# Performance work log

Measured on AMD Instinct MI355X. Metric: run time of the kernel, lower is better.

Reference implementation:

```python
import jax, jax.numpy as jnp
import numpy as np

DT = 0.1
WHEELBASE = 2.8
STATE_DIM = 12


def setup_inputs() -> dict:
    key = jax.random.key(0)
    k1, k2, k3 = jax.random.split(key, 3)
    b, l, h = 512, 64, 80
    x0 = jax.random.normal(k1, (b, STATE_DIM), dtype=jnp.float32)
    controls = jax.random.normal(k2, (b, l, h, 3), dtype=jnp.float32)
    deg = jax.random.uniform(k3, (b, 5), dtype=jnp.float32)
    return {"x0": x0, "controls": controls, "deg": deg}


def reference(x0, controls, deg):
    b, l, h, _ = controls.shape
    # degradation scales, broadcast over the l (candidate) dim: [b, 1]
    steer_scale = jnp.maximum(deg[:, 0:1], 0.05)
    brake_scale = jnp.maximum(deg[:, 1:2], 0.05)
    throttle_scale = jnp.maximum(deg[:, 2:3], 0.05)
    friction = jnp.maximum(deg[:, 4:5], 0.1)

    x_init = jnp.broadcast_to(x0[:, None, :], (b, l, x0.shape[-1]))  # [b,l,12]

    def step(x, u):  # x: [b,l,12], u: [b,l,3]
        delta = steer_scale * jnp.tanh(u[..., 0])
        fb = brake_scale * jax.nn.sigmoid(u[..., 1])
        fx = throttle_scale * jax.nn.sigmoid(u[..., 2])
        px, py, psi, vx, vy = (x[..., 0], x[..., 1], x[..., 2], x[..., 3], x[..., 4])
        speed = jnp.sqrt(vx * vx + vy * vy + 1e-06)
        acc = jnp.minimum(jnp.maximum(2.8 * fx - 6.5 * fb, -7.5 * friction), 3.0)
        speed2 = jnp.maximum(speed + acc * DT, 0.0)
        tan_d = jnp.tan(jnp.clip(delta, -0.75, 0.75))
        raw_yaw = speed2 / WHEELBASE * tan_d
        yaw_lim = jnp.maximum(friction * 9.81 / jnp.maximum(speed2, 2.0), 0.15)
        yaw_rate = jnp.clip(raw_yaw, -1.0, 1.0) * yaw_lim
        beta = jnp.clip(jnp.arctan(0.45 * tan_d), -0.65, 0.65)
        psi2 = psi + yaw_rate * DT
        vx2 = speed2 * jnp.cos(psi2 + beta)
        vy2 = speed2 * jnp.sin(psi2 + beta)
        px2 = px + vx2 * DT
        py2 = py + vy2 * DT
        ax = (vx2 - vx) / DT
        ay = (vy2 - vy) / DT
        x2 = jnp.stack([px2, py2, psi2, vx2, vy2, yaw_rate, ax, ay, beta, delta, fb, fx], -1)
        return x2, x2

    controls_t = jnp.moveaxis(controls, 2, 0)  # [h,b,l,3]
    _, traj = jax.lax.scan(step, x_init, controls_t)  # traj: [h,b,l,12]
    traj = jnp.concatenate([x_init[None], traj], axis=0)  # [h+1,b,l,12]
    return jnp.moveaxis(traj, 0, 2)  # [b,l,h+1,12]
```

## Files before the change

### kernel.cpp

```cpp
#include <hip/hip_runtime.h>
#include <math.h>


#define N_B 512
#define N_L 64
#define N_H 80
#define DT_F 0.1f
#define PITCH_F4 25
#define CPITCH 7
#define SPC 8
#define NCH 10
#define INV2PI 0.15915494309189535f

__device__ __forceinline__ float fast_rcp(float x) { return __builtin_amdgcn_rcpf(x); }

__device__ __forceinline__ float fast_tanh(float x) {
    const float e2 = __expf(2.0f * x);
    return (e2 - 1.0f) * fast_rcp(e2 + 1.0f);
}

__device__ __forceinline__ float fast_sigmoid(float x) {
    return fast_rcp(1.0f + __expf(-x));
}

__device__ __forceinline__ float fast_atan_small(float z) {
    const float z2 = z * z;
    float p = 1.0f / 9.0f;
    p = fmaf(p, z2, -1.0f / 7.0f);
    p = fmaf(p, z2, 1.0f / 5.0f);
    p = fmaf(p, z2, -1.0f / 3.0f);
    p = fmaf(p, z2, 1.0f);
    return z * p;
}

__device__ __forceinline__ float fast_tan_075(float x) {
    const float x2 = x * x;
    float p = 0.0035916f;
    p = fmaf(p, x2, 0.0088632f);
    p = fmaf(p, x2, 0.0218695f);
    p = fmaf(p, x2, 0.0539683f);
    p = fmaf(p, x2, 0.1333333f);
    p = fmaf(p, x2, 0.3333333f);
    return fmaf(p * x2, x, x);
}

struct Ctl { float delta, fb, fx, tan_d, beta, acc; };

__device__ __forceinline__ Ctl make_ctl(float u0, float u1, float u2,
                                        float steer_scale, float brake_scale,
                                        float throttle_scale, float neg_brake_lim) {
    Ctl t;
    t.delta = steer_scale * fast_tanh(u0);
    t.fb = brake_scale    * fast_sigmoid(u1);
    t.fx = throttle_scale * fast_sigmoid(u2);
    const float dc = fminf(fmaxf(t.delta, -0.75f), 0.75f);
    t.tan_d = fast_tan_075(dc);
    t.beta = fminf(fmaxf(fast_atan_small(0.45f * t.tan_d), -0.65f), 0.65f);
    t.acc = fminf(fmaxf(2.8f * t.fx - 6.5f * t.fb, neg_brake_lim), 3.0f);
    return t;
}

__global__ __launch_bounds__(128) void degraded_bicycle_rollout_kernel(
    const float* __restrict__ x0,
    const float* __restrict__ controls,
    const float* __restrict__ deg,
    float* __restrict__ out)
{
    __shared__ float4 lds4[2][N_L * PITCH_F4];
    __shared__ float4 ldsc[2][N_L * CPITCH];

    const int lane = threadIdx.x & 63;
    const int wave = threadIdx.x >> 6;
    const int b = blockIdx.x;

    const size_t out_b = (size_t)b * 62208;

#define FLUSH_SLICE(FBUF, FC)                                                     \
    {                                                                             \
        const size_t obase = out_b + 12 + (size_t)(FC) * (SPC * 12);              \
        _Pragma("unroll")                                                         \
        for (int i = 0; i < 24; ++i) {                                            \
            const unsigned flat = i * 64 + lane;                                  \
            const unsigned l = flat / 24u;                                        \
            const unsigned q = flat - l * 24u;                                    \
            const float4 v = lds4[FBUF][l * PITCH_F4 + q];                        \
            *reinterpret_cast<float4*>(out + obase + (size_t)l * 972 + q * 4) = v;\
        }                                                                         \
    }

#define CTL_L(i) (((i) * 64u + (unsigned)lane) / 6u)
#define CTL_J(i) (((i) * 64u + (unsigned)lane) - CTL_L(i) * 6u)

    if (wave == 0) {
        const float* dg = deg + b * 5;
        const float steer_scale    = fmaxf(dg[0], 0.05f);
        const float brake_scale    = fmaxf(dg[1], 0.05f);
        const float throttle_scale = fmaxf(dg[2], 0.05f);
        const float friction       = fmaxf(dg[4], 0.1f);

        const float4* x0v = reinterpret_cast<const float4*>(x0 + b * 12);
        const float4 xi0 = x0v[0];
        const float4 xi1 = x0v[1];

        float px  = xi0.x;
        float py  = xi0.y;
        float psi = xi0.z;
        float vxp = xi0.w;
        float vyp = xi1.x;
        float s = __builtin_amdgcn_sqrtf(fmaf(vxp, vxp, fmaf(vyp, vyp, 1e-6f)));

        const float neg_brake_lim = -7.5f * friction;
        const float yaw_num = friction * 9.81f;
        const float inv_wheelbase = 1.0f / 2.8f;

        __syncthreads();

        for (int c = 0; c < NCH; ++c) {
            float4* lrow = &lds4[c & 1][lane * PITCH_F4];
            const float4* crow = &ldsc[c & 1][lane * CPITCH];

            const float4 u0 = crow[0];
            const float4 u1 = crow[1];
            const float4 u2 = crow[2];
            const float4 u3 = crow[3];
            const float4 u4 = crow[4];
            const float4 u5 = crow[5];

            const Ctl tA = make_ctl(u0.x, u0.y, u0.z, steer_scale, brake_scale, throttle_scale, neg_brake_lim);
            const Ctl tB = make_ctl(u0.w, u1.x, u1.y, steer_scale, brake_scale, throttle_scale, neg_brake_lim);
            const Ctl tC = make_ctl(u1.z, u1.w, u2.x, steer_scale, brake_scale, throttle_scale, neg_brake_lim);
            const Ctl tD = make_ctl(u2.y, u2.z, u2.w, steer_scale, brake_scale, throttle_scale, neg_brake_lim);
            const Ctl tE = make_ctl(u3.x, u3.y, u3.z, steer_scale, brake_scale, throttle_scale, neg_brake_lim);
            const Ctl tF = make_ctl(u3.w, u4.x, u4.y, steer_scale, brake_scale, throttle_scale, neg_brake_lim);
            const Ctl tG = make_ctl(u4.z, u4.w, u5.x, steer_scale, brake_scale, throttle_scale, neg_brake_lim);
            const Ctl tH = make_ctl(u5.y, u5.z, u5.w, steer_scale, brake_scale, throttle_scale, neg_brake_lim);

#define ROLL_STEP(T, RR)                                                          \
            {                                                                     \
                const float s2 = fmaxf(fmaf((T).acc, DT_F, s), 0.0f);             \
                const float raw_yaw = s2 * inv_wheelbase * (T).tan_d;             \
                const float yaw_lim = fmaxf(yaw_num * fast_rcp(fmaxf(s2, 2.0f)), 0.15f); \
                const float yaw_rate = fminf(fmaxf(raw_yaw, -1.0f), 1.0f) * yaw_lim; \
                const float psi2 = fmaf(yaw_rate, DT_F, psi);                     \
                const float ang = (psi2 + (T).beta) * INV2PI;                     \
                const float sn = __builtin_amdgcn_sinf(ang);                      \
                const float cs = __builtin_amdgcn_cosf(ang);                      \
                const float vx2 = s2 * cs;                                        \
                const float vy2 = s2 * sn;                                        \
                const float px2 = fmaf(vx2, DT_F, px);                            \
                const float py2 = fmaf(vy2, DT_F, py);                            \
                const float ax = (vx2 - vxp) * 10.0f;                             \
                const float ay = (vy2 - vyp) * 10.0f;                             \
                lrow[(RR) * 3 + 0] = make_float4(px2, py2, psi2, vx2);            \
                lrow[(RR) * 3 + 1] = make_float4(vy2, yaw_rate, ax, ay);          \
                lrow[(RR) * 3 + 2] = make_float4((T).beta, (T).delta, (T).fb, (T).fx); \
                s = __builtin_amdgcn_sqrtf(fmaf(s2, s2, 1e-6f));                  \
                px = px2; py = py2; psi = psi2; vxp = vx2; vyp = vy2;             \
            }

            ROLL_STEP(tA, 0) ROLL_STEP(tB, 1) ROLL_STEP(tC, 2) ROLL_STEP(tD, 3)
            ROLL_STEP(tE, 4) ROLL_STEP(tF, 5) ROLL_STEP(tG, 6) ROLL_STEP(tH, 7)
#undef ROLL_STEP

            __syncthreads();
        }
    } else {
        {
            const float4* x0v = reinterpret_cast<const float4*>(x0 + b * 12);
            const float4 xq0 = x0v[0];
            const float4 xq1 = x0v[1];
            const float4 xq2 = x0v[2];
            #pragma unroll
            for (int i = 0; i < 3; ++i) {
                const unsigned flat = i * 64 + lane;
                const unsigned l = flat / 3u;
                const unsigned q = flat - l * 3u;
                const float4 v = (q == 0) ? xq0 : (q == 1) ? xq1 : xq2;
                *reinterpret_cast<float4*>(out + out_b + (size_t)l * 972 + q * 4) = v;
            }
        }
        {
            const size_t gbase = (size_t)b * 15360;
            float4 q0 = *reinterpret_cast<const float4*>(controls + gbase + (size_t)CTL_L(0) * 240 + CTL_J(0) * 4);
            float4 q1 = *reinterpret_cast<const float4*>(controls + gbase + (size_t)CTL_L(1) * 240 + CTL_J(1) * 4);
            float4 q2 = *reinterpret_cast<const float4*>(controls + gbase + (size_t)CTL_L(2) * 240 + CTL_J(2) * 4);
            float4 q3 = *reinterpret_cast<const float4*>(controls + gbase + (size_t)CTL_L(3) * 240 + CTL_J(3) * 4);
            float4 q4 = *reinterpret_cast<const float4*>(controls + gbase + (size_t)CTL_L(4) * 240 + CTL_J(4) * 4);
            float4 q5 = *reinterpret_cast<const float4*>(controls + gbase + (size_t)CTL_L(5) * 240 + CTL_J(5) * 4);
            ldsc[0][CTL_L(0) * CPITCH + CTL_J(0)] = q0;
            ldsc[0][CTL_L(1) * CPITCH + CTL_J(1)] = q1;
            ldsc[0][CTL_L(2) * CPITCH + CTL_J(2)] = q2;
            ldsc[0][CTL_L(3) * CPITCH + CTL_J(3)] = q3;
            ldsc[0][CTL_L(4) * CPITCH + CTL_J(4)] = q4;
            ldsc[0][CTL_L(5) * CPITCH + CTL_J(5)] = q5;
        }
        asm volatile("s_waitcnt lgkmcnt(0)" ::: "memory");
        __builtin_amdgcn_s_barrier();
        __builtin_amdgcn_sched_barrier(0);

        for (int c = 0; c < NCH; ++c) {
            float4 q0, q1, q2, q3, q4, q5;
            const bool more = (c + 1 < NCH);
            if (more) {
                const size_t gbase = (size_t)b * 15360 + (size_t)(c + 1) * 24;
                q0 = *reinterpret_cast<const float4*>(controls + gbase + (size_t)CTL_L(0) * 240 + CTL_J(0) * 4);
                q1 = *reinterpret_cast<const float4*>(controls + gbase + (size_t)CTL_L(1) * 240 + CTL_J(1) * 4);
                q2 = *reinterpret_cast<const float4*>(controls + gbase + (size_t)CTL_L(2) * 240 + CTL_J(2) * 4);
                q3 = *reinterpret_cast<const float4*>(controls + gbase + (size_t)CTL_L(3) * 240 + CTL_J(3) * 4);
                q4 = *reinterpret_cast<const float4*>(controls + gbase + (size_t)CTL_L(4) * 240 + CTL_J(4) * 4);
                q5 = *reinterpret_cast<const float4*>(controls + gbase + (size_t)CTL_L(5) * 240 + CTL_J(5) * 4);
            }
            if (c > 0) FLUSH_SLICE((c - 1) & 1, c - 1)
            if (more) {
                const int nb = (c + 1) & 1;
                ldsc[nb][CTL_L(0) * CPITCH + CTL_J(0)] = q0;
                ldsc[nb][CTL_L(1) * CPITCH + CTL_J(1)] = q1;
                ldsc[nb][CTL_L(2) * CPITCH + CTL_J(2)] = q2;
                ldsc[nb][CTL_L(3) * CPITCH + CTL_J(3)] = q3;
                ldsc[nb][CTL_L(4) * CPITCH + CTL_J(4)] = q4;
                ldsc[nb][CTL_L(5) * CPITCH + CTL_J(5)] = q5;
            }
            asm volatile("s_waitcnt lgkmcnt(0)" ::: "memory");
            __builtin_amdgcn_s_barrier();
            __builtin_amdgcn_sched_barrier(0);
        }
        FLUSH_SLICE((NCH - 1) & 1, NCH - 1)
    }
#undef FLUSH_SLICE
#undef CTL_L
#undef CTL_J
}

extern "C" void kernel_launch(void* const* d_in, const int* in_sizes, int n_in,
                              void* d_out, int out_size, void* d_ws, size_t ws_size,
                              hipStream_t stream) {
    (void)in_sizes; (void)n_in; (void)d_ws; (void)ws_size; (void)out_size;
    const float* x0       = (const float*)d_in[0];
    const float* controls = (const float*)d_in[1];
    const float* deg      = (const float*)d_in[2];
    float* out            = (float*)d_out;

    dim3 grid(N_B), block(128);
    hipLaunchKernelGGL(degraded_bicycle_rollout_kernel, grid, block, 0, stream,
                       x0, controls, deg, out);
}
```

Baseline: 35.40 us.

## Split output flush across three helper waves with 256-thread blocks

Raises the block from two waves to four. Wave 0 still runs the sequential rollout. Wave 1 prefetches controls and flushes the first third of each finished output slice, while waves 2 and 3 flush the remaining two thirds, with wave 2 also writing the initial state. The aim is to spread the global store traffic per slice across more waves so the flush keeps pace with the compute wave. In exchange it adds more waves per block and block-wide barriers with more participants, which could reduce occupancy or lengthen barrier waits.

```diff
diff --git a/kernel.cpp b/kernel.cpp
--- a/kernel.cpp
+++ b/kernel.cpp
@@ -60,7 +60,7 @@
     return t;
 }
 
-__global__ __launch_bounds__(128) void degraded_bicycle_rollout_kernel(
+__global__ __launch_bounds__(256) void degraded_bicycle_rollout_kernel(
     const float* __restrict__ x0,
     const float* __restrict__ controls,
     const float* __restrict__ deg,
@@ -70,16 +70,16 @@
     __shared__ float4 ldsc[2][N_L * CPITCH];
 
     const int lane = threadIdx.x & 63;
-    const int wave = threadIdx.x >> 6;
+    const int wv   = threadIdx.x >> 6;
     const int b = blockIdx.x;
 
     const size_t out_b = (size_t)b * 62208;
 
-#define FLUSH_SLICE(FBUF, FC)                                                     \
+#define FLUSH_SLICE(FBUF, FC, I0, I1)                                             \
     {                                                                             \
         const size_t obase = out_b + 12 + (size_t)(FC) * (SPC * 12);              \
         _Pragma("unroll")                                                         \
-        for (int i = 0; i < 24; ++i) {                                            \
+        for (int i = (I0); i < (I1); ++i) {                                       \
             const unsigned flat = i * 64 + lane;                                  \
             const unsigned l = flat / 24u;                                        \
             const unsigned q = flat - l * 24u;                                    \
@@ -91,7 +91,7 @@
 #define CTL_L(i) (((i) * 64u + (unsigned)lane) / 6u)
 #define CTL_J(i) (((i) * 64u + (unsigned)lane) - CTL_L(i) * 6u)
 
-    if (wave == 0) {
+    if (wv == 0) {
         const float* dg = deg + b * 5;
         const float steer_scale    = fmaxf(dg[0], 0.05f);
         const float brake_scale    = fmaxf(dg[1], 0.05f);
@@ -164,8 +164,46 @@
 
             __syncthreads();
         }
+    } else if (wv == 1) {
+        {
+            const size_t gbase = (size_t)b * 15360;
+            #pragma unroll
+            for (int i = 0; i < 6; ++i) {
+                const float4 v = *reinterpret_cast<const float4*>(
+                    controls + gbase + (size_t)CTL_L(i) * 240 + CTL_J(i) * 4);
+                ldsc[0][CTL_L(i) * CPITCH + CTL_J(i)] = v;
+            }
+        }
+        __syncthreads();
+
+        for (int c = 0; c < NCH; ++c) {
+            float4 q0, q1, q2, q3, q4, q5;
+            const bool more = (c + 1 < NCH);
+            if (more) {
+                const size_t gbase = (size_t)b * 15360 + (size_t)(c + 1) * 24;
+                q0 = *reinterpret_cast<const float4*>(controls + gbase + (size_t)CTL_L(0) * 240 + CTL_J(0) * 4);
+                q1 = *reinterpret_cast<const float4*>(controls + gbase + (size_t)CTL_L(1) * 240 + CTL_J(1) * 4);
+                q2 = *reinterpret_cast<const float4*>(controls + gbase + (size_t)CTL_L(2) * 240 + CTL_J(2) * 4);
+                q3 = *reinterpret_cast<const float4*>(controls + gbase + (size_t)CTL_L(3) * 240 + CTL_J(3) * 4);
+                q4 = *reinterpret_cast<const float4*>(controls + gbase + (size_t)CTL_L(4) * 240 + CTL_J(4) * 4);
+                q5 = *reinterpret_cast<const float4*>(controls + gbase + (size_t)CTL_L(5) * 240 + CTL_J(5) * 4);
+            }
+            if (c > 0) FLUSH_SLICE((c - 1) & 1, c - 1, 0, 8)
+            if (more) {
+                const int nb = (c + 1) & 1;
+                ldsc[nb][CTL_L(0) * CPITCH + CTL_J(0)] = q0;
+                ldsc[nb][CTL_L(1) * CPITCH + CTL_J(1)] = q1;
+                ldsc[nb][CTL_L(2) * CPITCH + CTL_J(2)] = q2;
+                ldsc[nb][CTL_L(3) * CPITCH + CTL_J(3)] = q3;
+                ldsc[nb][CTL_L(4) * CPITCH + CTL_J(4)] = q4;
+                ldsc[nb][CTL_L(5) * CPITCH + CTL_J(5)] = q5;
+            }
+            __syncthreads();
+        }
+        FLUSH_SLICE((NCH - 1) & 1, NCH - 1, 0, 8)
     } else {
-        {
+        const int i0 = (wv - 1) * 8;
+        if (wv == 2) {
             const float4* x0v = reinterpret_cast<const float4*>(x0 + b * 12);
             const float4 xq0 = x0v[0];
             const float4 xq1 = x0v[1];
@@ -179,52 +217,13 @@
                 *reinterpret_cast<float4*>(out + out_b + (size_t)l * 972 + q * 4) = v;
             }
         }
-        {
-            const size_t gbase = (size_t)b * 15360;
-            float4 q0 = *reinterpret_cast<const float4*>(controls + gbase + (size_t)CTL_L(0) * 240 + CTL_J(0) * 4);
-            float4 q1 = *reinterpret_cast<const float4*>(controls + gbase + (size_t)CTL_L(1) * 240 + CTL_J(1) * 4);
-            float4 q2 = *reinterpret_cast<const float4*>(controls + gbase + (size_t)CTL_L(2) * 240 + CTL_J(2) * 4);
-            float4 q3 = *reinterpret_cast<const float4*>(controls + gbase + (size_t)CTL_L(3) * 240 + CTL_J(3) * 4);
-            float4 q4 = *reinterpret_cast<const float4*>(controls + gbase + (size_t)CTL_L(4) * 240 + CTL_J(4) * 4);
-            float4 q5 = *reinterpret_cast<const float4*>(controls + gbase + (size_t)CTL_L(5) * 240 + CTL_J(5) * 4);
-            ldsc[0][CTL_L(0) * CPITCH + CTL_J(0)] = q0;
-            ldsc[0][CTL_L(1) * CPITCH + CTL_J(1)] = q1;
-            ldsc[0][CTL_L(2) * CPITCH + CTL_J(2)] = q2;
-            ldsc[0][CTL_L(3) * CPITCH + CTL_J(3)] = q3;
-            ldsc[0][CTL_L(4) * CPITCH + CTL_J(4)] = q4;
-            ldsc[0][CTL_L(5) * CPITCH + CTL_J(5)] = q5;
-        }
-        asm volatile("s_waitcnt lgkmcnt(0)" ::: "memory");
-        __builtin_amdgcn_s_barrier();
-        __builtin_amdgcn_sched_barrier(0);
+        __syncthreads();
 
         for (int c = 0; c < NCH; ++c) {
-            float4 q0, q1, q2, q3, q4, q5;
-            const bool more = (c + 1 < NCH);
-            if (more) {
-                const size_t gbase = (size_t)b * 15360 + (size_t)(c + 1) * 24;
-                q0 = *reinterpret_cast<const float4*>(controls + gbase + (size_t)CTL_L(0) * 240 + CTL_J(0) * 4);
-                q1 = *reinterpret_cast<const float4*>(controls + gbase + (size_t)CTL_L(1) * 240 + CTL_J(1) * 4);
-                q2 = *reinterpret_cast<const float4*>(controls + gbase + (size_t)CTL_L(2) * 240 + CTL_J(2) * 4);
-                q3 = *reinterpret_cast<const float4*>(controls + gbase + (size_t)CTL_L(3) * 240 + CTL_J(3) * 4);
-                q4 = *reinterpret_cast<const float4*>(controls + gbase + (size_t)CTL_L(4) * 240 + CTL_J(4) * 4);
-                q5 = *reinterpret_cast<const float4*>(controls + gbase + (size_t)CTL_L(5) * 240 + CTL_J(5) * 4);
-            }
-            if (c > 0) FLUSH_SLICE((c - 1) & 1, c - 1)
-            if (more) {
-                const int nb = (c + 1) & 1;
-                ldsc[nb][CTL_L(0) * CPITCH + CTL_J(0)] = q0;
-                ldsc[nb][CTL_L(1) * CPITCH + CTL_J(1)] = q1;
-                ldsc[nb][CTL_L(2) * CPITCH + CTL_J(2)] = q2;
-                ldsc[nb][CTL_L(3) * CPITCH + CTL_J(3)] = q3;
-                ldsc[nb][CTL_L(4) * CPITCH + CTL_J(4)] = q4;
-                ldsc[nb][CTL_L(5) * CPITCH + CTL_J(5)] = q5;
-            }
-            asm volatile("s_waitcnt lgkmcnt(0)" ::: "memory");
-            __builtin_amdgcn_s_barrier();
-            __builtin_amdgcn_sched_barrier(0);
-        }
-        FLUSH_SLICE((NCH - 1) & 1, NCH - 1)
+            if (c > 0) FLUSH_SLICE((c - 1) & 1, c - 1, i0, i0 + 8)
+            __syncthreads();
+        }
+        FLUSH_SLICE((NCH - 1) & 1, NCH - 1, i0, i0 + 8)
     }
 #undef FLUSH_SLICE
 #undef CTL_L
@@ -240,7 +239,7 @@
     const float* deg      = (const float*)d_in[2];
     float* out            = (float*)d_out;
 
-    dim3 grid(N_B), block(128);
+    dim3 grid(N_B), block(256);
     hipLaunchKernelGGL(degraded_bicycle_rollout_kernel, grid, block, 0, stream,
                        x0, controls, deg, out);
 }
```

Result: no change. 35.86 us (+1.3%).
